# Optimization experiments

Hardware: AMD Instinct MI355X
Metric: run time of the kernel (lower is better)

The kernel has to match this reference:

```python
import jax, jax.numpy as jnp
import numpy as np

D, P, S, E = 200, 200, 150, 150  # drugs, proteins, diseases, side-effects
EMB = 256

def setup_inputs() -> dict:
    key = jax.random.key(0)
    ks = jax.random.split(key, 10)
    s = 0.05
    type_mask = jnp.concatenate([
        jnp.zeros(D, jnp.int64) if False else jnp.full((D,), 0, jnp.int32),
        jnp.full((P,), 1, jnp.int32),
        jnp.full((S,), 2, jnp.int32),
        jnp.full((E,), 3, jnp.int32)]).astype(jnp.int32)
    return {
        'type_mask': type_mask,
        'entity_embedding': jax.random.normal(ks[0], (D + P + S + E, EMB)) * s,
        'relation_embedding': jax.random.normal(ks[1], (1200, EMB)) * s,
        'W_ent': jax.random.normal(ks[2], (EMB, EMB)) * s,
        'W_rel': jax.random.normal(ks[3], (EMB, EMB)) * s,
        'W1': jax.random.normal(ks[4], (2 * EMB, 1024)) * s,
        'b1': jnp.zeros((1024,)),
        'W2': jax.random.normal(ks[5], (1024, 512)) * s,
        'b2': jnp.zeros((512,)),
        'W3': jax.random.normal(ks[6], (512, 2)) * s,
        'b3': jnp.zeros((2,)),
    }

def _pair_softmax(a, b, W1, b1, W2, b2, W3, b3):
    # classifier(concat(a[i], b[j])) for the full cartesian product.
    # First linear is decomposed: W1 @ [a;b] = a@W1a + b@W1b (same math,
    # avoids materializing the [Na*Nb, 2*EMB] concat tensor).
    W1a, W1b = W1[:EMB], W1[EMB:]
    ha = a @ W1a                      # [Na, 1024]
    hb = b @ W1b                      # [Nb, 1024]
    h = jax.nn.relu(ha[:, None, :] + hb[None, :, :] + b1)  # [Na, Nb, 1024]
    h = jax.nn.relu(h @ W2 + b2)      # [Na, Nb, 512]
    logits = h @ W3 + b3              # [Na, Nb, 2]
    Na, Nb = a.shape[0], b.shape[0]
    return jax.nn.softmax(logits.reshape(Na * Nb, 2), axis=-1)

def reference(type_mask, entity_embedding, relation_embedding, W_ent, W_rel,
              W1, b1, W2, b2, W3, b3):
    tm = np.asarray(type_mask)  # concrete, block-structured type ids
    idx = [np.nonzero(tm == t)[0] for t in range(4)]
    # project embeddings (project_on path; nn.Linear: x @ W)
    ent = entity_embedding @ W_ent
    _rel = relation_embedding @ W_rel  # computed in original forward, unused (graph_on off)
    drug, prot, dis, se = (ent[idx[0]], ent[idx[1]], ent[idx[2]], ent[idx[3]])
    cls = lambda a, b: _pair_softmax(a, b, W1, b1, W2, b2, W3, b3)
    out_dp = cls(drug, prot)
    out_dd = cls(drug, drug)
    out_ds = cls(drug, dis)
    out_de = cls(drug, se)
    out_ps = cls(prot, dis)
    out_pp = cls(prot, prot)
    out_pd = cls(prot, drug)
    out_ed = cls(se, drug)
    out_sp = cls(dis, prot)
    out_sd = cls(dis, drug)
    return (out_dp, out_dd, out_ds, out_de, out_ps, out_pp, out_pd,
            out_ed, out_sp, out_sd, drug)
```

## Files before the change

### kernel.cpp

```cpp
#include <hip/hip_runtime.h>
#include <hip/hip_bf16.h>

typedef __attribute__((ext_vector_type(4))) float floatx4;
typedef __attribute__((ext_vector_type(8))) __bf16 bf16x8;
typedef unsigned short ushort_t;

#define NENT  700
#define EMB   256
#define KDIM  1024
#define NDIM  512
#define HROWS 720
#define NPAIR 340000

#define WS_HA   0
#define WS_HB   (WS_HA + HROWS*KDIM*2)
#define WS_W2H  (WS_HB + HROWS*KDIM*2)
#define WS_ENT  (WS_W2H + NDIM*KDIM*2)
#define WS_LG   (WS_ENT + NENT*EMB*4)

__device__ __forceinline__ float ldin(const void* p, int i, int isbf) {
    return isbf ? __bfloat162float(((const __hip_bfloat16*)p)[i])
                : ((const float*)p)[i];
}

__device__ __forceinline__ int detect_bf16(const ushort_t* __restrict__ w) {
    int t = threadIdx.x & 63;
    int e = (w[2*t] >> 7) & 0xFF;
    unsigned long long m = __ballot(e >= 100 && e <= 126);
    return (__popcll(m) >= 48) ? 1 : 0;
}

#define LDS_BARRIER() do { __builtin_amdgcn_s_waitcnt(0xC07F); __builtin_amdgcn_s_barrier(); } while (0)

__global__ void prep_kernel(const void* __restrict__ E, const void* __restrict__ Went,
                            const void* __restrict__ W1, const void* __restrict__ b1,
                            const void* __restrict__ W2, __hip_bfloat16* __restrict__ W2H,
                            __hip_bfloat16* __restrict__ HA, __hip_bfloat16* __restrict__ HB,
                            void* __restrict__ out) {
    int isbf = detect_bf16((const ushort_t*)E);
    if (blockIdx.x < 720) {
        int part = blockIdx.x & 1;
        int ns   = (blockIdx.x >> 1) & 3;
        int rt   = blockIdx.x >> 3;
        int ib   = rt * 8;
        int t    = threadIdx.x;
        __shared__ float eL[8][EMB];
        __shared__ float rows[8][EMB];
#pragma unroll
        for (int r = 0; r < 8; ++r) {
            int i = ib + r;
            eL[r][t] = (i < NENT) ? ldin(E, i*EMB + t, isbf) : 0.f;
        }
        __syncthreads();
        float a8[8];
#pragma unroll
        for (int r = 0; r < 8; ++r) a8[r] = 0.f;
        if (isbf) {
            const __hip_bfloat16* W = (const __hip_bfloat16*)Went;
            for (int k = 0; k < EMB; ++k) {
                float w = __bfloat162float(W[k*EMB + t]);
#pragma unroll
                for (int r = 0; r < 8; ++r) a8[r] += eL[r][k] * w;
            }
        } else {
            const float* W = (const float*)Went;
            for (int k = 0; k < EMB; ++k) {
                float w = W[k*EMB + t];
#pragma unroll
                for (int r = 0; r < 8; ++r) a8[r] += eL[r][k] * w;
            }
        }
#pragma unroll
        for (int r = 0; r < 8; ++r) {
            rows[r][t] = a8[r];
            int i = ib + r;
            if (!part && !ns && i < 200) {
                if (isbf) ((__hip_bfloat16*)out)[680000 + i*EMB + t] = __float2bfloat16(a8[r]);
                else      ((float*)out)[680000 + i*EMB + t] = a8[r];
            }
        }
        __syncthreads();

        int n = ns*256 + t;
        float acc[8];
#pragma unroll
        for (int r = 0; r < 8; ++r) acc[r] = 0.f;
        int wbase = part*EMB*KDIM;
        if (isbf) {
            const __hip_bfloat16* W = (const __hip_bfloat16*)W1;
            for (int k = 0; k < EMB; ++k) {
                float w = __bfloat162float(W[wbase + k*KDIM + n]);
#pragma unroll
                for (int r = 0; r < 8; ++r) acc[r] += rows[r][k] * w;
            }
        } else {
            const float* W = (const float*)W1;
            for (int k = 0; k < EMB; ++k) {
                float w = W[wbase + k*KDIM + n];
#pragma unroll
                for (int r = 0; r < 8; ++r) acc[r] += rows[r][k] * w;
            }
        }
        __hip_bfloat16* HX = part ? HB : HA;
        float bv = part ? 0.f : ldin(b1, n, isbf);
#pragma unroll
        for (int r = 0; r < 8; ++r) {
            float v = acc[r];
            if (!part) v += bv;
            HX[(ib + r)*KDIM + n] = __float2bfloat16(v);
        }
    } else {
        int g = (blockIdx.x - 720)*256 + threadIdx.x;
        int lane = g & 63, f = (g >> 6) & 15, kc = (g >> 10) & 31, half = g >> 15;
        int l15 = lane & 15, quad = lane >> 4;
        int n = half*256 + f*16 + l15;
        bf16x8 v;
#pragma unroll
        for (int j = 0; j < 8; ++j) {
            int k = kc*32 + quad*8 + j;
            v[j] = (__bf16)ldin(W2, k*NDIM + n, isbf);
        }
        *(bf16x8*)(W2H + (size_t)g*8) = v;
    }
}

union U8 { bf16x8 v; unsigned u[4]; };

__device__ __forceinline__ bf16x8 mk_af3(bf16x8 ha, bf16x8 hb) {
    U8 r;
#pragma unroll
    for (int j = 0; j < 4; ++j) {
        float x0 = fmaxf((float)ha[2*j]   + (float)hb[2*j],   0.f);
        float x1 = fmaxf((float)ha[2*j+1] + (float)hb[2*j+1], 0.f);
        unsigned u0 = __float_as_uint(x0) + 0x8000u;
        unsigned u1 = __float_as_uint(x1) + 0x8000u;
#if defined(__has_builtin) && __has_builtin(__builtin_amdgcn_perm)
        r.u[j] = __builtin_amdgcn_perm(u1, u0, 0x07060302u);
#else
        r.u[j] = (u0 >> 16) | (u1 & 0xFFFF0000u);
#endif
    }
    return r.v;
}

#define MFMA(a, b, c) __builtin_amdgcn_mfma_f32_16x16x32_bf16((a), (b), (c), 0, 0, 0)

__global__ __launch_bounds__(256, 2) void pair_kernel(
        const ushort_t* __restrict__ HA, const ushort_t* __restrict__ HB,
        const ushort_t* __restrict__ W2H, const void* __restrict__ E,
        const void* __restrict__ b2, const void* __restrict__ W3,
        const void* __restrict__ b3, void* __restrict__ out) {

    const int blkEnd[10] = {650,1300,1800,2300,2800,3450,4100,4594,5088,5582};
    const int aB[10]  = {0,0,0,0,200,200,200,550,400,400};
    const int bB[10]  = {200,0,400,550,400,200,0,0,200,0};
    const int NaT[10] = {200,200,200,200,200,200,200,150,150,150};
    const int NbT[10] = {200,200,150,150,150,200,200,200,200,200};
    const int jTl[10] = {13,13,10,10,10,13,13,13,13,13};
    const int oOf[10] = {0,80000,160000,220000,280000,340000,420000,500000,560000,620000};

    __shared__ __align__(16) unsigned char sAF[16384];
    __shared__ float lgt[4][64][2];

    int bid = blockIdx.x;
    int ty = 0;
    while (bid >= blkEnd[ty]) ty++;
    int lb = bid - (ty ? blkEnd[ty-1] : 0);
    int jT = jTl[ty];
    int it = lb / jT;
    int jt = lb - it*jT;
    int i0 = aB[ty] + it*4;
    int j0 = bB[ty] + jt*16;

    int tid  = threadIdx.x;
    int lane = tid & 63;
    int w    = tid >> 6;
    int kcw  = w & 1;
    int mp   = (w >> 1) * 2;
    int l15  = lane & 15;
    int quad = lane >> 4;
    int kb   = (bid*7) & 31;

    const char* WB0 = (const char*)W2H + (size_t)(w*4)*1024 + lane*16;
    const char* WB1 = WB0 + (size_t)512*1024;
    const ushort_t* HBp  = HB + (j0 + l15)*KDIM + quad*8;
    const ushort_t* HAp0 = HA + (i0 + mp)*KDIM + quad*8;
    const ushort_t* HAp1 = HAp0 + KDIM;

    floatx4 acc[4][8];
#pragma unroll
    for (int mf = 0; mf < 4; ++mf)
#pragma unroll
        for (int hf = 0; hf < 8; ++hf) acc[mf][hf] = (floatx4){0.f,0.f,0.f,0.f};

    bf16x8 Bc[2][4], Bn[2][4];
    int k0 = kb, k1 = (kb + 1) & 31;
#pragma unroll
    for (int nf = 0; nf < 4; ++nf) {
        Bc[0][nf] = *(const bf16x8*)(WB0 + (size_t)k0*16384 + nf*1024);
        Bc[1][nf] = *(const bf16x8*)(WB1 + (size_t)k0*16384 + nf*1024);
        Bn[0][nf] = *(const bf16x8*)(WB0 + (size_t)k1*16384 + nf*1024);
        Bn[1][nf] = *(const bf16x8*)(WB1 + (size_t)k1*16384 + nf*1024);
    }
    int kg0 = (kb + kcw) & 31;
    bf16x8 ha0 = *(const bf16x8*)(HAp0 + kg0*32);
    bf16x8 ha1 = *(const bf16x8*)(HAp1 + kg0*32);
    bf16x8 hb  = *(const bf16x8*)(HBp + kg0*32);

#pragma unroll 1
    for (int ph = 0; ph < 16; ++ph) {
        char* sW = (char*)sAF + (ph & 1)*8192 + kcw*4096 + mp*1024 + lane*16;
        *(bf16x8*)(sW)        = mk_af3(ha0, hb);
        *(bf16x8*)(sW + 1024) = mk_af3(ha1, hb);
        int kgn = (kb + 2*ph + 2 + kcw) & 31;
        ha0 = *(const bf16x8*)(HAp0 + kgn*32);
        ha1 = *(const bf16x8*)(HAp1 + kgn*32);
        hb  = *(const bf16x8*)(HBp + kgn*32);
        LDS_BARRIER();

        const char* sR = (const char*)sAF + (ph & 1)*8192 + lane*16;
        int kn2 = (kb + 2*ph + 2) & 31;
        int kn3 = (kb + 2*ph + 3) & 31;
#pragma unroll
        for (int m = 0; m < 4; ++m) {
            bf16x8 a = *(const bf16x8*)(sR + m*1024);
#pragma unroll
            for (int hf = 0; hf < 8; ++hf)
                acc[m][hf] = MFMA(a, Bc[hf>>2][hf&3], acc[m][hf]);
        }
#pragma unroll
        for (int nf = 0; nf < 4; ++nf) {
            Bc[0][nf] = *(const bf16x8*)(WB0 + (size_t)kn2*16384 + nf*1024);
            Bc[1][nf] = *(const bf16x8*)(WB1 + (size_t)kn2*16384 + nf*1024);
        }
#pragma unroll
        for (int m = 0; m < 4; ++m) {
            bf16x8 a = *(const bf16x8*)(sR + 4096 + m*1024);
#pragma unroll
            for (int hf = 0; hf < 8; ++hf)
                acc[m][hf] = MFMA(a, Bn[hf>>2][hf&3], acc[m][hf]);
        }
#pragma unroll
        for (int nf = 0; nf < 4; ++nf) {
            Bn[0][nf] = *(const bf16x8*)(WB0 + (size_t)kn3*16384 + nf*1024);
            Bn[1][nf] = *(const bf16x8*)(WB1 + (size_t)kn3*16384 + nf*1024);
        }
    }

    int isbf = detect_bf16((const ushort_t*)E);
    float b2v[8], wa[8], wb[8];
#pragma unroll
    for (int hf = 0; hf < 8; ++hf) {
        int n = (hf >> 2)*256 + w*64 + (hf & 3)*16 + l15;
        b2v[hf] = ldin(b2, n, isbf);
        wa[hf]  = ldin(W3, 2*n, isbf);
        wb[hf]  = ldin(W3, 2*n+1, isbf);
    }
#pragma unroll
    for (int mf = 0; mf < 4; ++mf) {
        float s0[4] = {0.f,0.f,0.f,0.f};
        float s1[4] = {0.f,0.f,0.f,0.f};
#pragma unroll
        for (int hf = 0; hf < 8; ++hf) {
            floatx4 c = acc[mf][hf];
#pragma unroll
            for (int r = 0; r < 4; ++r) {
                float v = fmaxf(c[r] + b2v[hf], 0.f);
                s0[r] += v * wa[hf];
                s1[r] += v * wb[hf];
            }
        }
#pragma unroll
        for (int off = 1; off < 16; off <<= 1) {
#pragma unroll
            for (int r = 0; r < 4; ++r) {
                s0[r] += __shfl_xor(s0[r], off, 64);
                s1[r] += __shfl_xor(s1[r], off, 64);
            }
        }
        if (l15 == 0) {
#pragma unroll
            for (int r = 0; r < 4; ++r) {
                int p = mf*16 + quad*4 + r;
                lgt[w][p][0] = s0[r];
                lgt[w][p][1] = s1[r];
            }
        }
    }
    __syncthreads();

    if (tid < 64) {
        int p = tid;
        float l0 = lgt[0][p][0] + lgt[1][p][0] + lgt[2][p][0] + lgt[3][p][0];
        float l1 = lgt[0][p][1] + lgt[1][p][1] + lgt[2][p][1] + lgt[3][p][1];
        l0 += ldin(b3, 0, isbf);
        l1 += ldin(b3, 1, isbf);
        int pi = it*4 + (p >> 4), pj = jt*16 + (p & 15);
        if (pi < NaT[ty] && pj < NbT[ty]) {
            float mx = fmaxf(l0, l1);
            float e0 = __expf(l0 - mx), e1 = __expf(l1 - mx);
            float inv = 1.f / (e0 + e1);
            int o = oOf[ty] + (pi*NbT[ty] + pj)*2;
            if (isbf) {
                __hip_bfloat16* ob = (__hip_bfloat16*)out;
                ob[o]   = __float2bfloat16(e0 * inv);
                ob[o+1] = __float2bfloat16(e1 * inv);
            } else {
                float* of = (float*)out;
                of[o]   = e0 * inv;
                of[o+1] = e1 * inv;
            }
        }
    }
}

extern "C" void kernel_launch(void* const* d_in, const int* in_sizes, int n_in,
                              void* d_out, int out_size, void* d_ws, size_t ws_size,
                              hipStream_t stream) {
    const void* E    = d_in[1];
    const void* Went = d_in[3];
    const void* W1   = d_in[5];
    const void* b1   = d_in[6];
    const void* W2   = d_in[7];
    const void* b2   = d_in[8];
    const void* W3   = d_in[9];
    const void* b3   = d_in[10];

    char* ws = (char*)d_ws;
    __hip_bfloat16* HA   = (__hip_bfloat16*)(ws + WS_HA);
    __hip_bfloat16* HB   = (__hip_bfloat16*)(ws + WS_HB);
    __hip_bfloat16* W2H  = (__hip_bfloat16*)(ws + WS_W2H);

    prep_kernel<<<dim3(976), dim3(256), 0, stream>>>(E, Went, W1, b1, W2, W2H, HA, HB, d_out);
    pair_kernel<<<dim3(5582), dim3(256), 0, stream>>>((const ushort_t*)HA, (const ushort_t*)HB,
                                                      (const ushort_t*)W2H, E, b2, W3, b3, d_out);
}
```

Before: 453.5 us.

## Switch pair GEMM to 32x32x16 MFMA with reorganized W2 layout and warp split

Replaces the 16x16x32 bf16 MFMA tiling with 32x32x16 MFMA. W2 is repacked into a matching fragment layout, and the work is re-split so that each wave owns 128 output columns over all K instead of a K-half and N-half split. The aim is higher MFMA throughput per instruction and fewer operand reloads per output. In exchange, the epilogue cross-lane reduction grows to 5 shuffle steps over 16 values and register pressure rises, which could hurt occupancy.

```diff
diff --git a/kernel.cpp b/kernel.cpp
--- a/kernel.cpp
+++ b/kernel.cpp
@@ -2,6 +2,7 @@
 #include <hip/hip_bf16.h>
 
 typedef __attribute__((ext_vector_type(4))) float floatx4;
+typedef __attribute__((ext_vector_type(16))) float floatx16;
 typedef __attribute__((ext_vector_type(8))) __bf16 bf16x8;
 typedef unsigned short ushort_t;
 
@@ -111,14 +112,13 @@
         }
     } else {
         int g = (blockIdx.x - 720)*256 + threadIdx.x;
-        int lane = g & 63, f = (g >> 6) & 15, kc = (g >> 10) & 31, half = g >> 15;
-        int l15 = lane & 15, quad = lane >> 4;
-        int n = half*256 + f*16 + l15;
+        int lane = g & 63, g32 = (g >> 6) & 7, k16 = (g >> 9) & 63, half = g >> 15;
+        int n = half*256 + g32*32 + (lane & 31);
+        int kb = k16*16 + (lane >> 5)*8;
         bf16x8 v;
 #pragma unroll
         for (int j = 0; j < 8; ++j) {
-            int k = kc*32 + quad*8 + j;
-            v[j] = (__bf16)ldin(W2, k*NDIM + n, isbf);
+            v[j] = (__bf16)ldin(W2, (kb + j)*NDIM + n, isbf);
         }
         *(bf16x8*)(W2H + (size_t)g*8) = v;
     }
@@ -143,7 +143,7 @@
     return r.v;
 }
 
-#define MFMA(a, b, c) __builtin_amdgcn_mfma_f32_16x16x32_bf16((a), (b), (c), 0, 0, 0)
+#define MFMA32(a, b, c) __builtin_amdgcn_mfma_f32_32x32x16_bf16((a), (b), (c), 0, 0, 0)
 
 __global__ __launch_bounds__(256, 2) void pair_kernel(
         const ushort_t* __restrict__ HA, const ushort_t* __restrict__ HB,
@@ -175,115 +175,104 @@
     int tid  = threadIdx.x;
     int lane = tid & 63;
     int w    = tid >> 6;
-    int kcw  = w & 1;
-    int mp   = (w >> 1) * 2;
     int l15  = lane & 15;
-    int quad = lane >> 4;
-    int kb   = (bid*7) & 31;
-
-    const char* WB0 = (const char*)W2H + (size_t)(w*4)*1024 + lane*16;
-    const char* WB1 = WB0 + (size_t)512*1024;
-    const ushort_t* HBp  = HB + (j0 + l15)*KDIM + quad*8;
-    const ushort_t* HAp0 = HA + (i0 + mp)*KDIM + quad*8;
-    const ushort_t* HAp1 = HAp0 + KDIM;
-
-    floatx4 acc[4][8];
-#pragma unroll
-    for (int mf = 0; mf < 4; ++mf)
-#pragma unroll
-        for (int hf = 0; hf < 8; ++hf) acc[mf][hf] = (floatx4){0.f,0.f,0.f,0.f};
-
-    bf16x8 Bc[2][4], Bn[2][4];
-    int k0 = kb, k1 = (kb + 1) & 31;
-#pragma unroll
-    for (int nf = 0; nf < 4; ++nf) {
-        Bc[0][nf] = *(const bf16x8*)(WB0 + (size_t)k0*16384 + nf*1024);
-        Bc[1][nf] = *(const bf16x8*)(WB1 + (size_t)k0*16384 + nf*1024);
-        Bn[0][nf] = *(const bf16x8*)(WB0 + (size_t)k1*16384 + nf*1024);
-        Bn[1][nf] = *(const bf16x8*)(WB1 + (size_t)k1*16384 + nf*1024);
-    }
-    int kg0 = (kb + kcw) & 31;
-    bf16x8 ha0 = *(const bf16x8*)(HAp0 + kg0*32);
-    bf16x8 ha1 = *(const bf16x8*)(HAp1 + kg0*32);
-    bf16x8 hb  = *(const bf16x8*)(HBp + kg0*32);
+    int hi   = lane >> 5;
+    int kb16 = ((bid*7) & 31) * 2;
+
+    const char* WB = (const char*)W2H + (size_t)(w >> 1)*524288 + (size_t)((w & 1)*4)*1024 + lane*16;
+    const ushort_t* HBq  = HB + (j0 + l15)*KDIM + hi*8;
+    const ushort_t* HAq0 = HA + (i0 + ((lane >> 4) & 1))*KDIM + hi*8;
+    const ushort_t* HAq1 = HAq0 + 2*KDIM;
+
+    floatx16 acc[2][4];
+#pragma unroll
+    for (int mf = 0; mf < 2; ++mf)
+#pragma unroll
+        for (int nf = 0; nf < 4; ++nf)
+#pragma unroll
+            for (int r = 0; r < 16; ++r) acc[mf][nf][r] = 0.f;
+
+    bf16x8 B4[4][4];
+#pragma unroll
+    for (int s = 0; s < 4; ++s) {
+        int k16 = (kb16 + s) & 63;
+#pragma unroll
+        for (int nf = 0; nf < 4; ++nf)
+            B4[s][nf] = *(const bf16x8*)(WB + (size_t)k16*8192 + nf*1024);
+    }
+
+    int kg0 = (kb16 + w) & 63;
+    bf16x8 ha0 = *(const bf16x8*)(HAq0 + kg0*16);
+    bf16x8 ha1 = *(const bf16x8*)(HAq1 + kg0*16);
+    bf16x8 hb  = *(const bf16x8*)(HBq  + kg0*16);
 
 #pragma unroll 1
     for (int ph = 0; ph < 16; ++ph) {
-        char* sW = (char*)sAF + (ph & 1)*8192 + kcw*4096 + mp*1024 + lane*16;
+        char* sW = (char*)sAF + (ph & 1)*8192 + w*2048 + lane*16;
         *(bf16x8*)(sW)        = mk_af3(ha0, hb);
         *(bf16x8*)(sW + 1024) = mk_af3(ha1, hb);
-        int kgn = (kb + 2*ph + 2 + kcw) & 31;
-        ha0 = *(const bf16x8*)(HAp0 + kgn*32);
-        ha1 = *(const bf16x8*)(HAp1 + kgn*32);
-        hb  = *(const bf16x8*)(HBp + kgn*32);
+        int kgn = (kb16 + 4*ph + 4 + w) & 63;
+        ha0 = *(const bf16x8*)(HAq0 + kgn*16);
+        ha1 = *(const bf16x8*)(HAq1 + kgn*16);
+        hb  = *(const bf16x8*)(HBq  + kgn*16);
         LDS_BARRIER();
 
         const char* sR = (const char*)sAF + (ph & 1)*8192 + lane*16;
-        int kn2 = (kb + 2*ph + 2) & 31;
-        int kn3 = (kb + 2*ph + 3) & 31;
-#pragma unroll
-        for (int m = 0; m < 4; ++m) {
-            bf16x8 a = *(const bf16x8*)(sR + m*1024);
-#pragma unroll
-            for (int hf = 0; hf < 8; ++hf)
-                acc[m][hf] = MFMA(a, Bc[hf>>2][hf&3], acc[m][hf]);
-        }
+#pragma unroll
+        for (int s = 0; s < 4; ++s) {
+            bf16x8 a0 = *(const bf16x8*)(sR + s*2048);
+            bf16x8 a1 = *(const bf16x8*)(sR + s*2048 + 1024);
+#pragma unroll
+            for (int nf = 0; nf < 4; ++nf)
+                acc[0][nf] = MFMA32(a0, B4[s][nf], acc[0][nf]);
+#pragma unroll
+            for (int nf = 0; nf < 4; ++nf)
+                acc[1][nf] = MFMA32(a1, B4[s][nf], acc[1][nf]);
+            int k16n = (kb16 + 4*ph + 4 + s) & 63;
+#pragma unroll
+            for (int nf = 0; nf < 4; ++nf)
+                B4[s][nf] = *(const bf16x8*)(WB + (size_t)k16n*8192 + nf*1024);
+        }
+    }
+
+    int isbf = detect_bf16((const ushort_t*)E);
+    float b2v[4], wa[4], wb[4];
+#pragma unroll
+    for (int nf = 0; nf < 4; ++nf) {
+        int n = w*128 + nf*32 + (lane & 31);
+        b2v[nf] = ldin(b2, n, isbf);
+        wa[nf]  = ldin(W3, 2*n, isbf);
+        wb[nf]  = ldin(W3, 2*n+1, isbf);
+    }
+#pragma unroll
+    for (int mf2 = 0; mf2 < 2; ++mf2) {
+        float s0[16], s1[16];
+#pragma unroll
+        for (int r = 0; r < 16; ++r) { s0[r] = 0.f; s1[r] = 0.f; }
 #pragma unroll
         for (int nf = 0; nf < 4; ++nf) {
-            Bc[0][nf] = *(const bf16x8*)(WB0 + (size_t)kn2*16384 + nf*1024);
-            Bc[1][nf] = *(const bf16x8*)(WB1 + (size_t)kn2*16384 + nf*1024);
-        }
-#pragma unroll
-        for (int m = 0; m < 4; ++m) {
-            bf16x8 a = *(const bf16x8*)(sR + 4096 + m*1024);
-#pragma unroll
-            for (int hf = 0; hf < 8; ++hf)
-                acc[m][hf] = MFMA(a, Bn[hf>>2][hf&3], acc[m][hf]);
-        }
-#pragma unroll
-        for (int nf = 0; nf < 4; ++nf) {
-            Bn[0][nf] = *(const bf16x8*)(WB0 + (size_t)kn3*16384 + nf*1024);
-            Bn[1][nf] = *(const bf16x8*)(WB1 + (size_t)kn3*16384 + nf*1024);
-        }
-    }
-
-    int isbf = detect_bf16((const ushort_t*)E);
-    float b2v[8], wa[8], wb[8];
-#pragma unroll
-    for (int hf = 0; hf < 8; ++hf) {
-        int n = (hf >> 2)*256 + w*64 + (hf & 3)*16 + l15;
-        b2v[hf] = ldin(b2, n, isbf);
-        wa[hf]  = ldin(W3, 2*n, isbf);
-        wb[hf]  = ldin(W3, 2*n+1, isbf);
-    }
-#pragma unroll
-    for (int mf = 0; mf < 4; ++mf) {
-        float s0[4] = {0.f,0.f,0.f,0.f};
-        float s1[4] = {0.f,0.f,0.f,0.f};
-#pragma unroll
-        for (int hf = 0; hf < 8; ++hf) {
-            floatx4 c = acc[mf][hf];
-#pragma unroll
-            for (int r = 0; r < 4; ++r) {
-                float v = fmaxf(c[r] + b2v[hf], 0.f);
-                s0[r] += v * wa[hf];
-                s1[r] += v * wb[hf];
-            }
-        }
-#pragma unroll
-        for (int off = 1; off < 16; off <<= 1) {
-#pragma unroll
-            for (int r = 0; r < 4; ++r) {
+            floatx16 c = acc[mf2][nf];
+#pragma unroll
+            for (int r = 0; r < 16; ++r) {
+                float v = fmaxf(c[r] + b2v[nf], 0.f);
+                s0[r] += v * wa[nf];
+                s1[r] += v * wb[nf];
+            }
+        }
+#pragma unroll
+        for (int off = 1; off < 32; off <<= 1) {
+#pragma unroll
+            for (int r = 0; r < 16; ++r) {
                 s0[r] += __shfl_xor(s0[r], off, 64);
                 s1[r] += __shfl_xor(s1[r], off, 64);
             }
         }
-        if (l15 == 0) {
-#pragma unroll
-            for (int r = 0; r < 4; ++r) {
-                int p = mf*16 + quad*4 + r;
-                lgt[w][p][0] = s0[r];
-                lgt[w][p][1] = s1[r];
+        if ((lane & 31) == 0) {
+#pragma unroll
+            for (int r = 0; r < 16; ++r) {
+                int row = mf2*32 + (r & 3) + 8*(r >> 2) + 4*hi;
+                lgt[w][row][0] = s0[r];
+                lgt[w][row][1] = s1[r];
             }
         }
     }
```

Result: slower. 515.0 us (+13.6%).
